# Performance work log

Hardware: AMD Instinct MI355X
Metric: run time of the kernel (lower is better)

## Reference

```python
import jax, jax.numpy as jnp
import numpy as np
from jax.ops import segment_sum

N_NODES = 500000
N_EDGES = 1000000
N_GRAPHS = 20000
F_IN = 78


def gcn_conv(x, W, b, src, dst, n):
    # PyG GCNConv: add self-loops, symmetric normalization D^-1/2 A D^-1/2
    h = x @ W  # [N, Fout]
    deg = segment_sum(jnp.ones(src.shape[0], x.dtype), dst, num_segments=n) + 1.0  # self-loop
    dinv = jax.lax.rsqrt(deg)  # [N]
    norm = dinv[src] * dinv[dst]  # [E]
    agg = segment_sum(h[src] * norm[:, None], dst, num_segments=n)  # neighbor messages
    agg = agg + h * (dinv * dinv)[:, None]  # self-loop message
    return agg + b


def global_mean_pool(x, batch, n_graphs):
    s = segment_sum(x, batch, num_segments=n_graphs)
    cnt = segment_sum(jnp.ones(x.shape[0], x.dtype), batch, num_segments=n_graphs)
    return s / jnp.maximum(cnt, 1.0)[:, None]


def setup_inputs() -> dict:
    key = jax.random.key(0)
    ks = jax.random.split(key, 16)
    x = jax.random.normal(ks[0], (N_NODES, F_IN), dtype=jnp.float32)
    edge_index = jax.random.randint(ks[1], (2, N_EDGES), 0, N_NODES, dtype=jnp.int32)
    batch = jnp.sort(jax.random.randint(ks[2], (N_NODES,), 0, N_GRAPHS, dtype=jnp.int32))

    def lin(k, fi, fo):
        s = 1.0 / np.sqrt(fi)
        kw, kb = jax.random.split(k)
        return (jax.random.uniform(kw, (fi, fo), jnp.float32, -s, s),
                jax.random.uniform(kb, (fo,), jnp.float32, -s, s))

    W1, b1 = lin(ks[3], F_IN, F_IN)
    W2, b2 = lin(ks[4], F_IN, F_IN * 2)
    W3, b3 = lin(ks[5], F_IN * 2, F_IN * 4)
    fW1, fb1 = lin(ks[6], F_IN * 4, 1024)
    fW2, fb2 = lin(ks[7], 1024, 128)
    return {"x": x, "edge_index": edge_index, "batch": batch,
            "W1": W1, "b1": b1, "W2": W2, "b2": b2, "W3": W3, "b3": b3,
            "fW1": fW1, "fb1": fb1, "fW2": fW2, "fb2": fb2}


def reference(x, edge_index, batch, W1, b1, W2, b2, W3, b3, fW1, fb1, fW2, fb2):
    src, dst = edge_index[0], edge_index[1]
    n = x.shape[0]
    h = jax.nn.relu(gcn_conv(x, W1, b1, src, dst, n))
    h = jax.nn.relu(gcn_conv(h, W2, b2, src, dst, n))
    h = jax.nn.relu(gcn_conv(h, W3, b3, src, dst, n))
    g = global_mean_pool(h, batch, N_GRAPHS)  # [G, 312]
    g = jax.nn.relu(g @ fW1 + fb1)  # dropout is identity at eval
    return g @ fW2 + fb2
```

## Files before the change

### kernel.cpp

```cpp
#include <hip/hip_runtime.h>
#include <hip/hip_fp16.h>

#define N_NODES 500000
#define N_EDGES 1000000
#define N_GRAPHS 20000

typedef _Float16 f16x8 __attribute__((ext_vector_type(8)));
typedef float f32x4 __attribute__((ext_vector_type(4)));

__global__ __launch_bounds__(256) void fill_u32(unsigned* p, unsigned v, int n) {
  int i = blockIdx.x * 256 + threadIdx.x;
  if (i < n) p[i] = v;
}

__global__ __launch_bounds__(256) void hist_dst(const int* __restrict__ dst, int* cnt, int e) {
  int i = blockIdx.x * 256 + threadIdx.x;
  if (i < e) atomicAdd(&cnt[dst[i]], 1);
}

__global__ __launch_bounds__(256) void scanA(const int* __restrict__ deg, int* __restrict__ loc,
                                             int* __restrict__ partials, int n) {
  __shared__ int ts[256];
  int b = blockIdx.x, t = threadIdx.x;
  int base = b * 1024 + t * 4;
  int v[4], s = 0;
#pragma unroll
  for (int j = 0; j < 4; ++j) {
    v[j] = (base + j < n) ? deg[base + j] : 0;
    s += v[j];
  }
  ts[t] = s;
  __syncthreads();
  for (int off = 1; off < 256; off <<= 1) {
    int x = (t >= off) ? ts[t - off] : 0;
    __syncthreads();
    ts[t] += x;
    __syncthreads();
  }
  if (t == 255) partials[b] = ts[255];
  int run = ts[t] - s;
#pragma unroll
  for (int j = 0; j < 4; ++j) {
    if (base + j < n) loc[base + j] = run;
    run += v[j];
  }
}

__global__ __launch_bounds__(512) void scanB(int* partials, int nb) {
  __shared__ int s[512];
  int t = threadIdx.x;
  s[t] = (t < nb) ? partials[t] : 0;
  __syncthreads();
  if (t == 0) {
    int run = 0;
    for (int i = 0; i < nb; ++i) { int v = s[i]; s[i] = run; run += v; }
  }
  __syncthreads();
  if (t < nb) partials[t] = s[t];
}

__global__ __launch_bounds__(256) void scanC(int* __restrict__ rowptr, const int* __restrict__ partials,
                                             int* __restrict__ cur, int n, int e) {
  int i = blockIdx.x * 256 + threadIdx.x;
  if (i < n) {
    int v = rowptr[i] + partials[i >> 10];
    rowptr[i] = v;
    cur[i] = v;
  }
  if (i == 0) rowptr[n] = e;
}

__global__ __launch_bounds__(256) void dinv_k(const int* __restrict__ rowptr, float* dinv, int n) {
  int i = blockIdx.x * 256 + threadIdx.x;
  if (i < n) dinv[i] = rsqrtf(1.0f + (float)(rowptr[i + 1] - rowptr[i]));
}

__global__ __launch_bounds__(256) void bucket(const int* __restrict__ src, const int* __restrict__ dst,
                                              int* __restrict__ cur, int* __restrict__ ssrc, int e) {
  int i = blockIdx.x * 256 + threadIdx.x;
  if (i < e) ssrc[atomicAdd(&cur[dst[i]], 1)] = src[i];
}

__global__ __launch_bounds__(256) void ell_build(const int* __restrict__ rowptr,
                                                 const int* __restrict__ ssrc,
                                                 int4* __restrict__ ell, int n) {
  int i = blockIdx.x * 256 + threadIdx.x;
  if (i >= n) return;
  int r0 = rowptr[i], r1 = rowptr[i + 1];
  int deg = r1 - r0;
  int4 e;
  e.x = deg;
  e.y = (deg > 0) ? ssrc[r0] : 0;
  e.z = (deg > 1) ? ssrc[r0 + 1] : 0;
  e.w = (deg > 2) ? ssrc[r0 + 2] : 0;
  ell[i] = e;
}

__global__ __launch_bounds__(256) void graph_starts(const int* __restrict__ batch,
                                                    int* __restrict__ gstart, int n) {
  int i = blockIdx.x * 256 + threadIdx.x;
  if (i < n) {
    int b = batch[i];
    int bp = (i == 0) ? -1 : batch[i - 1];
    for (int g = bp + 1; g <= b; ++g) gstart[g] = i;
  } else if (i == n) {
    int bl = batch[n - 1];
    for (int g = bl + 1; g <= N_GRAPHS; ++g) gstart[g] = n;
  }
}

template <int CW>
__global__ __launch_bounds__(256) void wt_conv(const float* __restrict__ W, _Float16* __restrict__ WT,
                                               int K, int Nout, int ldw, int KP, int total) {
  int i = blockIdx.x * 256 + threadIdx.x;
  if (i >= total) return;
  int c = i / KP, kp = i - c * KP;
  int k; bool valid;
  if (CW) { int blk = kp / CW, r = kp - blk * CW; k = blk * 78 + r; valid = (r < 78) && (k < K); }
  else { k = kp; valid = kp < K; }
  WT[i] = (valid && c < Nout) ? (_Float16)W[(size_t)k * ldw + c] : (_Float16)0.f;
}

__global__ __launch_bounds__(256) void xconv(const float* __restrict__ xin,
                                             const float* __restrict__ dinv,
                                             _Float16* __restrict__ Xh) {
  unsigned idx = blockIdx.x * 256u + threadIdx.x;
  if (idx >= (unsigned)N_NODES * 48u) return;
  unsigned n = idx / 48u, c2 = idx - n * 48u;
  __half2 h = __floats2half2_rn(0.f, 0.f);
  if (c2 < 39u) {
    float di = dinv[n];
    float2 v = *reinterpret_cast<const float2*>(xin + (size_t)n * 78 + 2 * c2);
    h = __floats2half2_rn(v.x * di, v.y * di);
  }
  *reinterpret_cast<__half2*>((__half*)Xh + (size_t)n * 96 + 2 * c2) = h;
}

template <int KP, int OUT_MODE, int BLDS, int PLANE>
__global__ __launch_bounds__(256) void gemm_direct(
    const _Float16* __restrict__ in, const _Float16* __restrict__ WT,
    void* __restrict__ outp, const float* __restrict__ rs, const float* __restrict__ bo,
    int M, int Nout, int LDO, size_t planeStride) {
  constexpr int NS = KP / 32;
  constexpr bool HOIST = (NS <= 5);
  __shared__ _Float16 Bs[BLDS ? 5 * NS * 64 * 8 : 8];
  const int tid = threadIdx.x;
  const int lane = tid & 63;
  const int wid = tid >> 6;
  const int row0 = blockIdx.y * 128;
  const int col0 = PLANE ? 0 : blockIdx.x * 80;
  const _Float16* wt = WT + (size_t)(PLANE ? blockIdx.x * 78 : col0) * KP;
  const float* bop = PLANE ? bo + blockIdx.x * 78 : bo;
  _Float16* out16 = (_Float16*)outp + (PLANE ? (size_t)blockIdx.x * planeStride : 0);
  float* out32 = (float*)outp;
  const int koff = (lane >> 4) * 8;
  const int gr0 = row0 + wid * 32 + (lane & 15);
  const bool v0 = gr0 < M, v1 = (gr0 + 16) < M;
  const _Float16* a0 = in + (size_t)gr0 * KP + koff;
  const _Float16* a1 = a0 + (size_t)16 * KP;
  const _Float16* bp = wt + (size_t)(lane & 15) * KP + koff;

  if (BLDS) {
    for (int i = tid; i < 5 * NS * 64; i += 256) {
      int l = i & 63;
      int nf = (i >> 6) % 5;
      int s = i / 320;
      int r = nf * 16 + (l & 15);
      int k = s * 32 + ((l >> 4) << 3);
      *reinterpret_cast<uint4*>(&Bs[(size_t)i * 8]) =
          *reinterpret_cast<const uint4*>(wt + (size_t)r * KP + k);
    }
    __syncthreads();
  }

  const f16x8 zf = {0, 0, 0, 0, 0, 0, 0, 0};
  const f32x4 z4 = {0.f, 0.f, 0.f, 0.f};
  f32x4 acc[2][5];
#pragma unroll
  for (int a = 0; a < 2; ++a)
#pragma unroll
    for (int b = 0; b < 5; ++b) acc[a][b] = z4;

  if constexpr (HOIST) {
    f16x8 A0[NS], A1[NS];
#pragma unroll
    for (int s = 0; s < NS; ++s) {
      A0[s] = v0 ? *reinterpret_cast<const f16x8*>(a0 + s * 32) : zf;
      A1[s] = v1 ? *reinterpret_cast<const f16x8*>(a1 + s * 32) : zf;
    }
#pragma unroll
    for (int s = 0; s < NS; ++s) {
      f16x8 bf[5];
#pragma unroll
      for (int nf = 0; nf < 5; ++nf) {
        if (BLDS)
          bf[nf] = *reinterpret_cast<const f16x8*>(&Bs[((size_t)(s * 5 + nf) * 64 + lane) * 8]);
        else
          bf[nf] = *reinterpret_cast<const f16x8*>(bp + (size_t)nf * 16 * KP + s * 32);
      }
#pragma unroll
      for (int nf = 0; nf < 5; ++nf) {
        acc[0][nf] = __builtin_amdgcn_mfma_f32_16x16x32_f16(A0[s], bf[nf], acc[0][nf], 0, 0, 0);
        acc[1][nf] = __builtin_amdgcn_mfma_f32_16x16x32_f16(A1[s], bf[nf], acc[1][nf], 0, 0, 0);
      }
    }
  } else {
#pragma unroll
    for (int s = 0; s < NS; ++s) {
      f16x8 af0 = v0 ? *reinterpret_cast<const f16x8*>(a0 + s * 32) : zf;
      f16x8 af1 = v1 ? *reinterpret_cast<const f16x8*>(a1 + s * 32) : zf;
      f16x8 bf[5];
#pragma unroll
      for (int nf = 0; nf < 5; ++nf) {
        if (BLDS)
          bf[nf] = *reinterpret_cast<const f16x8*>(&Bs[((size_t)(s * 5 + nf) * 64 + lane) * 8]);
        else
          bf[nf] = *reinterpret_cast<const f16x8*>(bp + (size_t)nf * 16 * KP + s * 32);
      }
#pragma unroll
      for (int nf = 0; nf < 5; ++nf) {
        acc[0][nf] = __builtin_amdgcn_mfma_f32_16x16x32_f16(af0, bf[nf], acc[0][nf], 0, 0, 0);
        acc[1][nf] = __builtin_amdgcn_mfma_f32_16x16x32_f16(af1, bf[nf], acc[1][nf], 0, 0, 0);
      }
    }
  }

#pragma unroll
  for (int rf = 0; rf < 2; ++rf) {
#pragma unroll
    for (int j = 0; j < 4; ++j) {
      int gr = row0 + wid * 32 + rf * 16 + (lane >> 4) * 4 + j;
      if (gr >= M) continue;
      float sc = (OUT_MODE == 3) ? rs[gr] : 0.f;
#pragma unroll
      for (int nf = 0; nf < 5; ++nf) {
        int oc = col0 + nf * 16 + (lane & 15);
        if (oc >= Nout) continue;
        float v = acc[rf][nf][j];
        if (OUT_MODE == 1) {
          out16[(size_t)gr * LDO + oc] = (_Float16)fmaxf(v + bop[oc], 0.f);
        } else if (OUT_MODE == 3) {
          out16[(size_t)gr * LDO + oc] = (_Float16)(fmaxf(v + bop[oc], 0.f) * sc);
        } else {
          out32[(size_t)gr * LDO + oc] = v + bop[oc];
        }
      }
    }
  }
}

__device__ inline void acc8(float* a, uint4 v) {
  const __half2* h = reinterpret_cast<const __half2*>(&v);
#pragma unroll
  for (int j = 0; j < 4; ++j) {
    float2 f = __half22float2(h[j]);
    a[2 * j] += f.x;
    a[2 * j + 1] += f.y;
  }
}

template <int LDI>
__device__ inline void gather_sumT(float* a, const _Float16* hbase, unsigned n,
                                   const int4* __restrict__ ell,
                                   const int* __restrict__ rowptr,
                                   const int* __restrict__ ssrc) {
  int4 e = ell[n];
  const int deg = e.x;
  uint4 sv = *reinterpret_cast<const uint4*>(hbase + (size_t)n * LDI);
  uint4 g0, g1, g2;
  if (deg > 0) g0 = *reinterpret_cast<const uint4*>(hbase + (size_t)e.y * LDI);
  if (deg > 1) g1 = *reinterpret_cast<const uint4*>(hbase + (size_t)e.z * LDI);
  if (deg > 2) g2 = *reinterpret_cast<const uint4*>(hbase + (size_t)e.w * LDI);
  {
    const __half2* h = reinterpret_cast<const __half2*>(&sv);
#pragma unroll
    for (int j = 0; j < 4; ++j) {
      float2 f = __half22float2(h[j]);
      a[2 * j] = f.x;
      a[2 * j + 1] = f.y;
    }
  }
  if (deg > 0) acc8(a, g0);
  if (deg > 1) acc8(a, g1);
  if (deg > 2) acc8(a, g2);
  if (deg > 3) {
    int r = rowptr[n] + 3, r1 = r + deg - 3;
    for (; r + 2 <= r1; r += 2) {
      uint4 va = *reinterpret_cast<const uint4*>(hbase + (size_t)ssrc[r] * LDI);
      uint4 vb = *reinterpret_cast<const uint4*>(hbase + (size_t)ssrc[r + 1] * LDI);
      acc8(a, va);
      acc8(a, vb);
    }
    if (r < r1) {
      uint4 va = *reinterpret_cast<const uint4*>(hbase + (size_t)ssrc[r] * LDI);
      acc8(a, va);
    }
  }
}

template <int LDI, int NSUB>
__global__ __launch_bounds__(256) void aggregateZ(
    const _Float16* __restrict__ in, const int4* __restrict__ ell,
    const int* __restrict__ rowptr, const int* __restrict__ ssrc,
    const float* __restrict__ dinv, _Float16* __restrict__ outZ, int ldo) {
  unsigned idx = blockIdx.x * 256u + threadIdx.x;
  if (idx >= (unsigned)N_NODES * NSUB) return;
  unsigned n = idx / NSUB, sub = idx - n * NSUB;
  float a[8];
  gather_sumT<LDI>(a, in + sub * 8u, n, ell, rowptr, ssrc);
  float di = dinv[n];
  _Float16 ov[8];
#pragma unroll
  for (int j = 0; j < 8; ++j) ov[j] = (_Float16)(di * a[j]);
  *reinterpret_cast<uint4*>(outZ + (size_t)n * ldo + sub * 8u) =
      *reinterpret_cast<const uint4*>(ov);
}

__global__ __launch_bounds__(256) void pool_seq(
    const _Float16* __restrict__ in, const int* __restrict__ gstart,
    _Float16* __restrict__ GA, int inOff, int coffGA) {
  unsigned idx = blockIdx.x * 256u + threadIdx.x;
  if (idx >= (unsigned)N_GRAPHS * 10u) return;
  unsigned g = idx / 10u, q = idx - g * 10u;
  int n0 = gstart[g], n1 = gstart[g + 1];
  const _Float16* base = in + inOff + q * 8;
  float a[8] = {0.f, 0.f, 0.f, 0.f, 0.f, 0.f, 0.f, 0.f};
  float b2[8] = {0.f, 0.f, 0.f, 0.f, 0.f, 0.f, 0.f, 0.f};
  int n = n0;
  for (; n + 2 <= n1; n += 2) {
    uint4 va = *reinterpret_cast<const uint4*>(base + (size_t)n * 160);
    uint4 vb = *reinterpret_cast<const uint4*>(base + (size_t)(n + 1) * 160);
    acc8(a, va);
    acc8(b2, vb);
  }
  if (n < n1) {
    uint4 va = *reinterpret_cast<const uint4*>(base + (size_t)n * 160);
    acc8(a, va);
  }
  float gi = 1.0f / fmaxf((float)(n1 - n0), 1.0f);
  _Float16 ov[8];
#pragma unroll
  for (int j = 0; j < 8; ++j) ov[j] = (_Float16)((a[j] + b2[j]) * gi);
  *reinterpret_cast<uint4*>(GA + (size_t)g * 320 + coffGA + q * 8) =
      *reinterpret_cast<const uint4*>(ov);
}

extern "C" void kernel_launch(void* const* d_in, const int* in_sizes, int n_in,
                              void* d_out, int out_size, void* d_ws, size_t ws_size,
                              hipStream_t stream) {
  const float* x   = (const float*)d_in[0];
  const int* ei    = (const int*)d_in[1];
  const int* batch = (const int*)d_in[2];
  const float* W1 = (const float*)d_in[3];
  const float* b1 = (const float*)d_in[4];
  const float* W2 = (const float*)d_in[5];
  const float* b2 = (const float*)d_in[6];
  const float* W3 = (const float*)d_in[7];
  const float* b3 = (const float*)d_in[8];
  const float* fW1 = (const float*)d_in[9];
  const float* fb1 = (const float*)d_in[10];
  const float* fW2 = (const float*)d_in[11];
  const float* fb2 = (const float*)d_in[12];
  float* out = (float*)d_out;

  const int Nn = N_NODES, E = N_EDGES, G = N_GRAPHS;
  const int* src = ei;
  const int* dst = ei + E;

  _Float16* A = (_Float16*)d_ws;
  _Float16* B = A + (size_t)Nn * 160;
  _Float16* GA = B + (size_t)Nn * 160;
  _Float16* W1T   = GA + (size_t)G * 320;
  _Float16* W2T   = W1T + 80 * 96;
  _Float16* W3T   = W2T + 160 * 96;
  _Float16* fW1T  = W3T + 320 * 160;
  _Float16* fW2T  = fW1T + (size_t)1040 * 320;
  float* dinv     = (float*)(fW2T + (size_t)160 * 1056);
  int* rowptr     = (int*)(dinv + Nn);
  int* cur        = rowptr + Nn + 1;
  int* ssrc       = cur + Nn;
  int* partials   = ssrc + E;
  int* gstart     = partials + 512;
  int4* ell = (int4*)(((uintptr_t)(gstart + G + 1) + 15) & ~(uintptr_t)15);

  _Float16* Xh = A;
  _Float16* Z1 = B;
  _Float16* H1 = A;
  _Float16* Z2 = B;
  _Float16* H2 = A;
  _Float16* Z3 = B;
  _Float16* O3 = A;
  _Float16* fc1 = B;

  dim3 blk(256);
  const int gN10 = (int)(((unsigned)Nn * 10u + 255u) / 256u);
  const int gN20 = (int)(((unsigned)Nn * 20u + 255u) / 256u);
  const int gG10 = (int)(((unsigned)G * 10u + 255u) / 256u);
  const dim3 nodeGrid(1, (Nn + 127) / 128);
  const dim3 pairGrid(2, (Nn + 127) / 128);
  const int NB = (Nn + 1023) / 1024;

  fill_u32<<<(Nn + 255) / 256, blk, 0, stream>>>((unsigned*)cur, 0u, Nn);
  hist_dst<<<(E + 255) / 256, blk, 0, stream>>>(dst, cur, E);
  scanA<<<NB, blk, 0, stream>>>(cur, rowptr, partials, Nn);
  scanB<<<1, 512, 0, stream>>>(partials, NB);
  scanC<<<(Nn + 255) / 256, blk, 0, stream>>>(rowptr, partials, cur, Nn, E);
  dinv_k<<<(Nn + 255) / 256, blk, 0, stream>>>(rowptr, dinv, Nn);
  bucket<<<(E + 255) / 256, blk, 0, stream>>>(src, dst, cur, ssrc, E);
  ell_build<<<(Nn + 255) / 256, blk, 0, stream>>>(rowptr, ssrc, ell, Nn);
  graph_starts<<<(Nn + 256) / 256, blk, 0, stream>>>(batch, gstart, Nn);

  wt_conv<0><<<(80 * 96 + 255) / 256, blk, 0, stream>>>(W1, W1T, 78, 78, 78, 96, 80 * 96);
  wt_conv<0><<<(160 * 96 + 255) / 256, blk, 0, stream>>>(W2, W2T, 78, 156, 156, 96, 160 * 96);
  wt_conv<80><<<(320 * 160 + 255) / 256, blk, 0, stream>>>(W3, W3T, 156, 312, 312, 160, 320 * 160);
  wt_conv<80><<<(1040 * 320 + 255) / 256, blk, 0, stream>>>(fW1, fW1T, 312, 1024, 1024, 320, 1040 * 320);
  wt_conv<0><<<(160 * 1056 + 255) / 256, blk, 0, stream>>>(fW2, fW2T, 1024, 128, 128, 1056, 160 * 1056);

  xconv<<<(int)(((unsigned)Nn * 48u + 255u) / 256u), blk, 0, stream>>>(x, dinv, Xh);

  aggregateZ<96, 10><<<gN10, blk, 0, stream>>>(Xh, ell, rowptr, ssrc, dinv, Z1, 96);
  gemm_direct<96, 3, 1, 0><<<nodeGrid, blk, 0, stream>>>(Z1, W1T, H1, dinv, b1, Nn, 78, 96, 0);

  aggregateZ<96, 10><<<gN10, blk, 0, stream>>>(H1, ell, rowptr, ssrc, dinv, Z2, 96);
  gemm_direct<96, 3, 1, 1><<<pairGrid, blk, 0, stream>>>(Z2, W2T, H2, dinv, b2, Nn, 78, 160, 80);

  aggregateZ<160, 20><<<gN20, blk, 0, stream>>>(H2, ell, rowptr, ssrc, dinv, Z3, 160);
  for (int p = 0; p < 2; ++p) {
    gemm_direct<160, 1, 1, 1><<<pairGrid, blk, 0, stream>>>(
        Z3, W3T + (size_t)(156 * p) * 160, O3, nullptr, b3 + 156 * p, Nn, 78, 160, 80);
    pool_seq<<<gG10, blk, 0, stream>>>(O3, gstart, GA, 0, (2 * p) * 80);
    pool_seq<<<gG10, blk, 0, stream>>>(O3, gstart, GA, 80, (2 * p + 1) * 80);
  }

  {
    dim3 g((1024 + 79) / 80, (G + 127) / 128);
    gemm_direct<320, 1, 1, 0><<<g, blk, 0, stream>>>(GA, fW1T, fc1, nullptr, fb1, G, 1024, 1056, 0);
  }
  {
    dim3 g((128 + 79) / 80, (G + 127) / 128);
    gemm_direct<1056, 2, 0, 0><<<g, blk, 0, stream>>>(fc1, fW2T, out, nullptr, fb2, G, 128, 128, 0);
  }
}
```

Measured before the change: 1.093 ms.

## Stage GEMM output tile through LDS for vectorized stores and hoist A loads

In the LDS-weight GEMM variants with fp16 output, the epilogue now writes the 128x80 result tile into shared memory and then copies it out with 16-byte row stores, replacing scattered 2-byte global writes. The hoisted A-fragment loads are also moved ahead of the shared-memory weight fill, so their global latency overlaps the LDS setup. This adds two extra barriers and a larger shared-memory allocation, which may lower occupancy. Out-of-range columns are now written as zeros, which relies on the padded output layout.

```diff
diff --git a/kernel.cpp b/kernel.cpp
--- a/kernel.cpp
+++ b/kernel.cpp
@@ -143,7 +143,11 @@
     int M, int Nout, int LDO, size_t planeStride) {
   constexpr int NS = KP / 32;
   constexpr bool HOIST = (NS <= 5);
-  __shared__ _Float16 Bs[BLDS ? 5 * NS * 64 * 8 : 8];
+  constexpr bool TSTORE = (BLDS != 0) && (OUT_MODE != 2);
+  constexpr int BS_BYTES = BLDS ? 5 * NS * 64 * 16 : 16;
+  constexpr int SM_BYTES = TSTORE ? (BS_BYTES > 20480 ? BS_BYTES : 20480) : BS_BYTES;
+  __shared__ __align__(16) char smem[SM_BYTES];
+  _Float16* Bs = (_Float16*)smem;
   const int tid = threadIdx.x;
   const int lane = tid & 63;
   const int wid = tid >> 6;
@@ -160,6 +164,19 @@
   const _Float16* a1 = a0 + (size_t)16 * KP;
   const _Float16* bp = wt + (size_t)(lane & 15) * KP + koff;
 
+  const f16x8 zf = {0, 0, 0, 0, 0, 0, 0, 0};
+  const f32x4 z4 = {0.f, 0.f, 0.f, 0.f};
+
+  f16x8 A0[HOIST ? NS : 1], A1[HOIST ? NS : 1];
+  if constexpr (HOIST) {
+#pragma unroll
+    for (int s = 0; s < NS; ++s) {
+      A0[s] = v0 ? *reinterpret_cast<const f16x8*>(a0 + s * 32) : zf;
+      A1[s] = v1 ? *reinterpret_cast<const f16x8*>(a1 + s * 32) : zf;
+    }
+    __builtin_amdgcn_sched_barrier(0);
+  }
+
   if (BLDS) {
     for (int i = tid; i < 5 * NS * 64; i += 256) {
       int l = i & 63;
@@ -173,8 +190,6 @@
     __syncthreads();
   }
 
-  const f16x8 zf = {0, 0, 0, 0, 0, 0, 0, 0};
-  const f32x4 z4 = {0.f, 0.f, 0.f, 0.f};
   f32x4 acc[2][5];
 #pragma unroll
   for (int a = 0; a < 2; ++a)
@@ -182,12 +197,6 @@
     for (int b = 0; b < 5; ++b) acc[a][b] = z4;
 
   if constexpr (HOIST) {
-    f16x8 A0[NS], A1[NS];
-#pragma unroll
-    for (int s = 0; s < NS; ++s) {
-      A0[s] = v0 ? *reinterpret_cast<const f16x8*>(a0 + s * 32) : zf;
-      A1[s] = v1 ? *reinterpret_cast<const f16x8*>(a1 + s * 32) : zf;
-    }
 #pragma unroll
     for (int s = 0; s < NS; ++s) {
       f16x8 bf[5];
@@ -225,24 +234,57 @@
     }
   }
 
-#pragma unroll
-  for (int rf = 0; rf < 2; ++rf) {
-#pragma unroll
-    for (int j = 0; j < 4; ++j) {
-      int gr = row0 + wid * 32 + rf * 16 + (lane >> 4) * 4 + j;
-      if (gr >= M) continue;
-      float sc = (OUT_MODE == 3) ? rs[gr] : 0.f;
-#pragma unroll
-      for (int nf = 0; nf < 5; ++nf) {
-        int oc = col0 + nf * 16 + (lane & 15);
-        if (oc >= Nout) continue;
-        float v = acc[rf][nf][j];
-        if (OUT_MODE == 1) {
-          out16[(size_t)gr * LDO + oc] = (_Float16)fmaxf(v + bop[oc], 0.f);
-        } else if (OUT_MODE == 3) {
-          out16[(size_t)gr * LDO + oc] = (_Float16)(fmaxf(v + bop[oc], 0.f) * sc);
-        } else {
-          out32[(size_t)gr * LDO + oc] = v + bop[oc];
+  if constexpr (TSTORE) {
+    __syncthreads();
+    _Float16* Os = (_Float16*)smem;
+#pragma unroll
+    for (int rf = 0; rf < 2; ++rf) {
+#pragma unroll
+      for (int j = 0; j < 4; ++j) {
+        int rl = wid * 32 + rf * 16 + (lane >> 4) * 4 + j;
+        int gr = row0 + rl;
+        float sc = (OUT_MODE == 3 && gr < M) ? rs[gr] : 0.f;
+#pragma unroll
+        for (int nf = 0; nf < 5; ++nf) {
+          int cl = nf * 16 + (lane & 15);
+          int oc = col0 + cl;
+          float r = 0.f;
+          if (oc < Nout) {
+            r = fmaxf(acc[rf][nf][j] + bop[oc], 0.f);
+            if (OUT_MODE == 3) r *= sc;
+          }
+          Os[rl * 80 + cl] = (_Float16)r;
+        }
+      }
+    }
+    __syncthreads();
+    for (int i = tid; i < 1280; i += 256) {
+      int rl = i / 10, u = i - rl * 10;
+      int gr = row0 + rl;
+      if (gr < M)
+        *reinterpret_cast<uint4*>(&out16[(size_t)gr * LDO + col0 + u * 8]) =
+            *reinterpret_cast<const uint4*>(&Os[rl * 80 + u * 8]);
+    }
+  } else {
+#pragma unroll
+    for (int rf = 0; rf < 2; ++rf) {
+#pragma unroll
+      for (int j = 0; j < 4; ++j) {
+        int gr = row0 + wid * 32 + rf * 16 + (lane >> 4) * 4 + j;
+        if (gr >= M) continue;
+        float sc = (OUT_MODE == 3) ? rs[gr] : 0.f;
+#pragma unroll
+        for (int nf = 0; nf < 5; ++nf) {
+          int oc = col0 + nf * 16 + (lane & 15);
+          if (oc >= Nout) continue;
+          float v = acc[rf][nf][j];
+          if (OUT_MODE == 1) {
+            out16[(size_t)gr * LDO + oc] = (_Float16)fmaxf(v + bop[oc], 0.f);
+          } else if (OUT_MODE == 3) {
+            out16[(size_t)gr * LDO + oc] = (_Float16)(fmaxf(v + bop[oc], 0.f) * sc);
+          } else {
+            out32[(size_t)gr * LDO + oc] = v + bop[oc];
+          }
         }
       }
     }
```

Result: faster. 1.020 ms (-6.6%).
